# Optimization experiments

Measured on AMD Instinct MI355X. Metric: run time of the kernel, lower is better.

## Reference

```python
import jax, jax.numpy as jnp
import numpy as np
from jax import lax

K = 5          # dynamic kernel size
GROUPS = 8     # inter_channels // group_channels = 128 // 16
R = 2          # pixel shuffle upscale factor
SLOPE = 0.01   # LeakyReLU default negative_slope
EPS = 1e-5     # BatchNorm eps


def conv2d(x, w, b, pad=0):
    # x: [B,C,H,W], w: [O,I,kh,kw]
    y = lax.conv_general_dilated(x, w, (1, 1), [(pad, pad), (pad, pad)],
                                 dimension_numbers=('NCHW', 'OIHW', 'NCHW'))
    return y + b[None, :, None, None]


def pixel_shuffle(x, r):
    B, C, H, W = x.shape
    x = x.reshape(B, C // (r * r), r, r, H, W)
    x = x.transpose(0, 1, 4, 2, 5, 3)  # B, C', H, r, W, r
    return x.reshape(B, C // (r * r), H * r, W * r)


def involution(x, weight, k, groups, pad):
    # x: [B,C,H,W]; weight: [B,groups,k,k,H,W]
    # out[b, g*gc+c, h, w] = sum_ij weight[b,g,i,j,h,w] * x_pad[b, g*gc+c, h+i, w+j]
    B, C, H, W = x.shape
    gc = C // groups
    xp = jnp.pad(x, ((0, 0), (0, 0), (pad, pad), (pad, pad)))
    xg = xp.reshape(B, groups, gc, H + 2 * pad, W + 2 * pad)
    out = jnp.zeros((B, groups, gc, H, W), x.dtype)
    for i in range(k):
        for j in range(k):
            out = out + weight[:, :, None, i, j] * xg[:, :, :, i:i + H, j:j + W]
    return out.reshape(B, C, H, W)


def setup_inputs() -> dict:
    key = jax.random.key(0)
    ks = jax.random.split(key, 16)
    s = 0.05
    return {
        'high_level': jax.random.normal(ks[0], (8, 128, 64, 64), jnp.float32),
        'low_level': jax.random.normal(ks[1], (8, 224, 128, 128), jnp.float32),
        'emb': jax.random.normal(ks[2], (8, 256, 128, 128), jnp.float32),
        'reduce_w': jax.random.normal(ks[3], (128, 256, 1, 1), jnp.float32) * s,
        'reduce_b': jax.random.normal(ks[4], (128,), jnp.float32) * s,
        'conv1_w': jax.random.normal(ks[5], (32, 128, 1, 1), jnp.float32) * s,
        'conv1_b': jax.random.normal(ks[6], (32,), jnp.float32) * s,
        'conv2_w': jax.random.normal(ks[7], (200, 32, 3, 3), jnp.float32) * s,
        'conv2_b': jax.random.normal(ks[8], (200,), jnp.float32) * s,
        'embconv_w': jax.random.normal(ks[9], (32, 256, 1, 1), jnp.float32) * s,
        'embconv_b': jax.random.normal(ks[10], (32,), jnp.float32) * s,
        'out_w': jax.random.normal(ks[11], (64, 128, 1, 1), jnp.float32) * s,
        'out_b': jax.random.normal(ks[12], (64,), jnp.float32) * s,
        'bn_gamma': jnp.ones((64,), jnp.float32),
        'bn_beta': jnp.zeros((64,), jnp.float32),
        'bn_mean': jnp.zeros((64,), jnp.float32),
        'bn_var': jax.random.uniform(ks[13], (64,), jnp.float32, 0.5, 1.5),
    }


def reference(high_level, low_level, emb,
              reduce_w, reduce_b, conv1_w, conv1_b, conv2_w, conv2_b,
              embconv_w, embconv_b, out_w, out_b,
              bn_gamma, bn_beta, bn_mean, bn_var):
    cat = jnp.concatenate([pixel_shuffle(high_level, R), low_level], axis=1)
    cat = conv2d(cat, reduce_w, reduce_b)
    mix = jax.nn.leaky_relu(conv2d(cat, conv1_w, conv1_b)
                            + conv2d(emb, embconv_w, embconv_b), SLOPE)
    w = conv2d(mix, conv2_w, conv2_b, pad=1)  # [B, K*K*GROUPS, H, W]
    B, _, H, W = w.shape
    w = w.reshape(B, GROUPS, K, K, H, W)
    o = involution(cat, w, K, GROUPS, (K - 1) // 2)
    o = conv2d(o, out_w, out_b)
    o = (o - bn_mean[None, :, None, None]) * (bn_gamma[None, :, None, None]
        / jnp.sqrt(bn_var[None, :, None, None] + EPS)) + bn_beta[None, :, None, None]
    return jax.nn.leaky_relu(o, SLOPE)
```

## Files before the change

### kernel.cpp

```cpp
#include <hip/hip_runtime.h>

typedef unsigned short u16; typedef unsigned int u32; typedef unsigned long long u64;
typedef __attribute__((ext_vector_type(8))) short short8;
typedef __attribute__((ext_vector_type(16))) float f32x16;

#define HW 16384

#define RED_B  0
#define C1E_B  128
#define C2_B   160
#define OUT_B  416
#define BN_SC  480
#define BN_SH  544
#define FLAG_OFF   4096
#define RWB_OFF    8192
#define C1B_OFF    73728
#define EMBB_OFF   81920
#define OUTB_OFF   98304
#define C2PB_OFF   114688
#define CAT2_OFF   524288
#define MIX_OFF    34078720
#define WGT_OFF    42467328

__device__ __forceinline__ float bf2f(u16 x){ u32 u=((u32)x)<<16; float f; __builtin_memcpy(&f,&u,4); return f; }
__device__ __forceinline__ u16 f2bf(float f){ u32 u; __builtin_memcpy(&u,&f,4); return (u16)((u + 0x7fffu + ((u>>16)&1u))>>16); }
__device__ __forceinline__ float lrelu(float x){ return x>0.f ? x : 0.01f*x; }

template<int M> __device__ __forceinline__ u16 ldb(const void* p, size_t i){
    if (M==1) return ((const u16*)p)[i];
    return f2bf(((const float*)p)[i]);
}
template<int M> __device__ __forceinline__ float ldf(const void* p, size_t i){
    if (M==1) return bf2f(((const u16*)p)[i]);
    return ((const float*)p)[i];
}
template<int M> __device__ __forceinline__ short8 ld8(const void* p, size_t i){
    short8 v;
    if (M==1){ __builtin_memcpy(&v, (const u16*)p + i, 16); }
    else {
        float a[8]; __builtin_memcpy(a, (const float*)p + i, 32);
#pragma unroll
        for (int r=0;r<8;r++) v[r] = (short)f2bf(a[r]);
    }
    return v;
}
template<int M> __device__ __forceinline__ void ld4(const void* p, size_t i, u32* d){
    if (M==1){ __builtin_memcpy(d, (const u16*)p + i, 8); }
    else {
        float a[4]; __builtin_memcpy(a, (const float*)p + i, 16);
        d[0] = (u32)f2bf(a[0]) | ((u32)f2bf(a[1])<<16);
        d[1] = (u32)f2bf(a[2]) | ((u32)f2bf(a[3])<<16);
    }
}
__device__ __forceinline__ void stA(u16* At, int stride, int p, int c, u16 v){
    At[p*stride + ((((c>>3) ^ ((p>>1)&7)))<<3) + (c&7)] = v;
}
__device__ __forceinline__ int swz(int p){ return ((p>>1) ^ (p>>3)) & 7; }

__global__ void detect_kernel(const void* __restrict__ emb, u32* __restrict__ flag){
    int tid = threadIdx.x;
    const u16* p = (const u16*)emb;
    int e = (p[tid*2] >> 7) & 0xFF;
    u64 m = __ballot(e >= 100 && e <= 140);
    if (tid == 0) *flag = (__popcll(m) >= 32) ? 1u : 0u;
}

template<int M>
__global__ __launch_bounds__(256) void k_prep(
    const void* rw, const void* rb, const void* c1w, const void* c1b,
    const void* c2w, const void* c2b, const void* ew, const void* eb,
    const void* ow, const void* ob, const void* gam, const void* bet,
    const void* mn, const void* vr, char* ws, const u32* flag)
{
    if (*flag != (u32)M) return;
    float* wf = (float*)ws;
    int i = blockIdx.x*256 + threadIdx.x;
    if (i < 32768) {
        int o = i>>8, ic = i&255;
        int s = ic>>4, qq = (ic>>3)&1, e = ic&7;
        int dst = (((o>>5)*16 + s)*64 + qq*32 + (o&31))*8 + e;
        ((u16*)(ws+RWB_OFF))[dst] = ldb<M>(rw, i);
    }
    else if (i < 36864)  ((u16*)(ws+C1B_OFF))[i-32768] = ldb<M>(c1w, i-32768);
    else if (i < 45056)  ((u16*)(ws+EMBB_OFF))[i-36864] = ldb<M>(ew, i-36864);
    else if (i < 53248)  ((u16*)(ws+OUTB_OFF))[i-45056] = ldb<M>(ow, i-45056);
    else if (i < 126976) {
        int j = i-53248; int o = j/288, k = j - o*288;
        int tap = k>>5, ic = k&31;
        u16 v = 0;
        if (o < 200) v = ldb<M>(c2w, (size_t)o*288 + ic*9 + tap);
        ((u16*)(ws+C2PB_OFF))[j] = v;
    }
    else if (i < 127584) {
        int j = i-126976;
        if (j < 128) wf[RED_B+j] = ldf<M>(rb, j);
        else if (j < 160) wf[C1E_B+j-128] = ldf<M>(c1b, j-128) + ldf<M>(eb, j-128);
        else if (j < 416) { int o = j-160; wf[C2_B+o] = (o<200) ? ldf<M>(c2b,o) : 0.f; }
        else if (j < 480) wf[OUT_B+j-416] = ldf<M>(ob, j-416);
        else if (j < 544) { int c=j-480; wf[BN_SC+c] = ldf<M>(gam,c) * rsqrtf(ldf<M>(vr,c)+1e-5f); }
        else { int c=j-544; wf[BN_SH+c] = ldf<M>(bet,c) - ldf<M>(mn,c)*ldf<M>(gam,c)*rsqrtf(ldf<M>(vr,c)+1e-5f); }
    }
}

template<int M>
__global__ __launch_bounds__(256) void k_reduce(
    const void* __restrict__ hi, const void* __restrict__ lo,
    const u16* __restrict__ rwB, const float* __restrict__ wf,
    u16* __restrict__ cat2, const u32* __restrict__ flag)
{
    if (*flag != (u32)M) return;
    __shared__ u16 At[64*264];
    const int tid = threadIdx.x, wvi = tid>>6, lane = tid&63;
    const int rt = (wvi>>1)*32, nc0 = (wvi&1)*64;
    const int col = lane&31, q = lane>>5;

    const int gpx = blockIdx.x*64;
    const int b = gpx>>14, p0 = gpx&16383;
    const int h = p0>>7, w0 = p0&127;

    const int co = tid>>3, po = tid&7;
    u32 W[8][4];
    if (co < 28) {
        u32 R[8][4];
#pragma unroll
        for (int j=0;j<8;j++){
            short8 v = ld8<M>(lo, ((size_t)(b*224 + 8*co + j))*HW + p0 + 8*po);
            __builtin_memcpy(&R[j][0], &v, 16);
        }
#pragma unroll
        for (int p=0;p<8;p++){
            const int u = p>>1, hf = p&1;
#pragma unroll
            for (int m=0;m<4;m++){
                u32 A0 = R[2*m][u], A1 = R[2*m+1][u];
                W[p][m] = hf ? ((A0>>16) | (A1 & 0xffff0000u))
                             : ((A0 & 0xffffu) | (A1<<16));
            }
        }
        const int ch = co + 4;
#pragma unroll
        for (int p=0;p<8;p++){
            int pg = 8*po + p;
            __builtin_memcpy(At + pg*264 + ((ch ^ swz(pg))<<3), &W[p][0], 16);
        }
    } else {
        const int cc0 = (co-28)*8, h2 = (h&1)*2;
        u32 E[8][2], O[8][2];
#pragma unroll
        for (int j=0;j<8;j++){
            int hc = (cc0+j)*4 + h2;
            size_t src = ((size_t)(b*128 + hc))*4096 + (size_t)(h>>1)*64 + (w0>>1) + 4*po;
            ld4<M>(hi, src,        E[j]);
            ld4<M>(hi, src + 4096, O[j]);
        }
#pragma unroll
        for (int p=0;p<8;p++){
            const int k = p>>1, u = k>>1, hf = k&1;
#pragma unroll
            for (int m=0;m<4;m++){
                u32 A0, A1;
                if (p&1){ A0 = O[2*m][u]; A1 = O[2*m+1][u]; }
                else    { A0 = E[2*m][u]; A1 = E[2*m+1][u]; }
                W[p][m] = hf ? ((A0>>16) | (A1 & 0xffff0000u))
                             : ((A0 & 0xffffu) | (A1<<16));
            }
        }
        const int ch = co - 28;
#pragma unroll
        for (int p=0;p<8;p++){
            int pg = 8*po + p;
            __builtin_memcpy(At + pg*264 + ((ch ^ swz(pg))<<3), &W[p][0], 16);
        }
    }
    __syncthreads();

    const int pp = rt + col, sw = swz(pp);
    const u16* arow = At + pp*264;
    const int ot0 = (wvi&1)*2;

    f32x16 acc0, acc1;
#pragma unroll
    for (int r=0;r<16;r++){ acc0[r]=0.f; acc1[r]=0.f; }

    short8 Bb[2][8];
#pragma unroll
    for (int nt=0;nt<2;nt++)
#pragma unroll
    for (int s=0;s<8;s++)
        __builtin_memcpy(&Bb[nt][s], rwB + (((size_t)((ot0+nt)*16 + s))*64 + lane)*8, 16);
#pragma unroll
    for (int s=0;s<8;s++){
        short8 a; __builtin_memcpy(&a, arow + (((2*s+q)^sw)<<3), 16);
        acc0 = __builtin_amdgcn_mfma_f32_32x32x16_bf16(a, Bb[0][s], acc0, 0,0,0);
        acc1 = __builtin_amdgcn_mfma_f32_32x32x16_bf16(a, Bb[1][s], acc1, 0,0,0);
    }
#pragma unroll
    for (int nt=0;nt<2;nt++)
#pragma unroll
    for (int s=0;s<8;s++)
        __builtin_memcpy(&Bb[nt][s], rwB + (((size_t)((ot0+nt)*16 + 8+s))*64 + lane)*8, 16);
#pragma unroll
    for (int s=8;s<16;s++){
        short8 a; __builtin_memcpy(&a, arow + (((2*s+q)^sw)<<3), 16);
        acc0 = __builtin_amdgcn_mfma_f32_32x32x16_bf16(a, Bb[0][s-8], acc0, 0,0,0);
        acc1 = __builtin_amdgcn_mfma_f32_32x32x16_bf16(a, Bb[1][s-8], acc1, 0,0,0);
    }

#pragma unroll
    for (int nt=0; nt<2; nt++){
        int oc = nc0 + nt*32 + col;
        float bias = wf[RED_B + oc];
#pragma unroll
        for (int r=0;r<16;r++){
            int row = (r&3) + 8*(r>>2) + 4*q;
            float v = (nt ? acc1[r] : acc0[r]) + bias;
            cat2[((size_t)(gpx + rt + row))*128 + oc] = f2bf(v);
        }
    }
}

template<int M>
__global__ __launch_bounds__(256) void k_mix(
    const u16* __restrict__ cat2, const void* __restrict__ emb,
    const u16* __restrict__ c1B, const u16* __restrict__ embB,
    const float* __restrict__ wf, u16* __restrict__ mixt, const u32* __restrict__ flag)
{
    if (*flag != (u32)M) return;
    __shared__ u16 At[128*136];
    const int tid = threadIdx.x, wvi = tid>>6, lane = tid&63;
    const int rt = wvi*32, col = lane&31, q = lane>>5;

    const int gpx = blockIdx.x*128;
    const int b = gpx>>14, p0 = gpx&16383;

    short8 Bc[8];
#pragma unroll
    for (int s=0;s<8;s++)  __builtin_memcpy(&Bc[s], c1B + (size_t)col*128 + s*16 + q*8, 16);

    f32x16 acc;
#pragma unroll
    for (int r=0;r<16;r++) acc[r]=0.f;
    const int pp = rt + col, sw = swz(pp);
    const u16* arow = At + pp*136;

#pragma unroll
    for (int i=0;i<8;i++){
        int idx = tid + i*256;
        int p = idx>>4, c16 = idx&15;
        short8 v;
        __builtin_memcpy(&v, cat2 + ((size_t)(gpx+p))*128 + c16*8, 16);
        *(short8*)(At + p*136 + ((c16 ^ swz(p))<<3)) = v;
    }
    __syncthreads();
#pragma unroll
    for (int s=0;s<8;s++){
        short8 a; __builtin_memcpy(&a, arow + (((2*s+q)^sw)<<3), 16);
        acc = __builtin_amdgcn_mfma_f32_32x32x16_bf16(a, Bc[s], acc, 0,0,0);
    }

    const int co = tid>>4, po = tid&15;
#pragma unroll 1
    for (int half=0; half<2; half++){
        u32 R[8][4];
#pragma unroll
        for (int j=0;j<8;j++){
            short8 v = ld8<M>(emb, ((size_t)(b*256 + half*128 + 8*co + j))*HW + p0 + 8*po);
            __builtin_memcpy(&R[j][0], &v, 16);
        }
        short8 Be[8];
#pragma unroll
        for (int s=0;s<8;s++)
            __builtin_memcpy(&Be[s], embB + (size_t)col*256 + half*128 + s*16 + q*8, 16);
        __syncthreads();
        u32 W[8][4];
#pragma unroll
        for (int p=0;p<8;p++){
            const int u = p>>1, hf = p&1;
#pragma unroll
            for (int m=0;m<4;m++){
                u32 A0 = R[2*m][u], A1 = R[2*m+1][u];
                W[p][m] = hf ? ((A0>>16) | (A1 & 0xffff0000u))
                             : ((A0 & 0xffffu) | (A1<<16));
            }
        }
#pragma unroll
        for (int p=0;p<8;p++){
            int pg = 8*po + p;
            __builtin_memcpy(At + pg*136 + ((co ^ swz(pg))<<3), &W[p][0], 16);
        }
        __syncthreads();
#pragma unroll
        for (int s=0;s<8;s++){
            short8 a; __builtin_memcpy(&a, arow + (((2*s+q)^sw)<<3), 16);
            acc = __builtin_amdgcn_mfma_f32_32x32x16_bf16(a, Be[s], acc, 0,0,0);
        }
    }
    float bias = wf[C1E_B + col];
#pragma unroll
    for (int r=0;r<16;r++){
        int row = (r&3) + 8*(r>>2) + 4*q;
        mixt[((size_t)(gpx + rt + row))*32 + col] = f2bf(lrelu(acc[r] + bias));
    }
}

__global__ __launch_bounds__(256) void k_conv2(
    const u16* __restrict__ mixt, const u16* __restrict__ c2B,
    const float* __restrict__ wf, u16* __restrict__ wgt)
{
    __shared__ u16 halo[100*32];
    const int tid = threadIdx.x, wvi = tid>>6, lane = tid&63;
    const int rt = (wvi>>1)*32, npair = wvi&1;
    const int nh = blockIdx.x & 1;
    const int nc0 = nh*128 + npair*64;
    const int col = lane&31, q = lane>>5;

    short8 B[2][18];
#pragma unroll
    for (int nt=0; nt<2; nt++){
        int o = nc0 + nt*32 + col;
#pragma unroll
        for (int s=0; s<18; s++)
            __builtin_memcpy(&B[nt][s], c2B + (size_t)o*288 + s*16 + q*8, 16);
    }

    for (int it=0; it<4; it++){
        int tile = (blockIdx.x>>1) + it*512;
        int b = tile>>8, tl = tile&255;
        int ty = tl>>4, tx = tl&15;
        __syncthreads();
#pragma unroll
        for (int i=0;i<2;i++){
            int idx = tid + i*256;
            if (idx < 400){
                int point = idx>>2, cq = idx&3;
                int y = ty*8 + point/10 - 1, x = tx*8 + point%10 - 1;
                short8 v;
                if (y>=0 && y<128 && x>=0 && x<128)
                    __builtin_memcpy(&v, mixt + ((size_t)(b*HW + y*128 + x))*32 + cq*8, 16);
                else { short z = 0; v = (short8){z,z,z,z,z,z,z,z}; }
                *(short8*)(halo + point*32 + cq*8) = v;
            }
        }
        __syncthreads();

        f32x16 acc0, acc1;
#pragma unroll
        for (int r=0;r<16;r++){ acc0[r]=0.f; acc1[r]=0.f; }
        int pp = rt + col, py = pp>>3, px = pp&7;
#pragma unroll
        for (int s=0;s<18;s++){
            int tap = s>>1, ih = s&1;
            int dy = tap/3, dx = tap%3;
            short8 a;
            __builtin_memcpy(&a, halo + ((py+dy)*10 + px+dx)*32 + ih*16 + q*8, 16);
            acc0 = __builtin_amdgcn_mfma_f32_32x32x16_bf16(a, B[0][s], acc0, 0,0,0);
            acc1 = __builtin_amdgcn_mfma_f32_32x32x16_bf16(a, B[1][s], acc1, 0,0,0);
        }
#pragma unroll
        for (int nt=0; nt<2; nt++){
            int oc = nc0 + nt*32 + col;
            if (oc < 200){
                float bias = wf[C2_B + oc];
#pragma unroll
                for (int r=0;r<16;r++){
                    int row = (r&3) + 8*(r>>2) + 4*q;
                    int p2 = rt + row;
                    int y = ty*8 + (p2>>3), x = tx*8 + (p2&7);
                    float v = (nt ? acc1[r] : acc0[r]) + bias;
                    wgt[((size_t)(b*200 + oc))*HW + y*128 + x] = f2bf(v);
                }
            }
        }
    }
}

template<int M>
__global__ __launch_bounds__(256) void k_inv(
    const u16* __restrict__ cat2, const u16* __restrict__ wgt,
    const u16* __restrict__ outB, const float* __restrict__ wf,
    void* __restrict__ out, const u32* __restrict__ flag)
{
    if (*flag != (u32)M) return;
    __shared__ u16 halo[400*16];
    __shared__ u16 og[256*16];
    const int tid = threadIdx.x, wvi = tid>>6, lane = tid&63;
    const int col = lane&31, q = lane>>5;
    const int b = blockIdx.y, ty = blockIdx.x>>3, tx = blockIdx.x&7;
    const int py = tid>>4, px = tid&15;
    const int h = ty*16 + py, w = tx*16 + px;

    f32x16 acc[2][2];
#pragma unroll
    for (int i=0;i<2;i++)
#pragma unroll
    for (int j=0;j<2;j++)
#pragma unroll
    for (int r=0;r<16;r++) acc[i][j][r] = 0.f;

#pragma unroll 1
    for (int g=0; g<8; g++){
        __syncthreads();
#pragma unroll
        for (int i=0;i<4;i++){
            int idx = tid + i*256;
            if (idx < 800){
                int point = idx>>1, cq = idx&1;
                int y = ty*16 + point/20 - 2, x = tx*16 + point%20 - 2;
                short8 v;
                if (y>=0 && y<128 && x>=0 && x<128)
                    __builtin_memcpy(&v, cat2 + ((size_t)(b*HW + y*128 + x))*128 + g*16 + cq*8, 16);
                else { short z=0; v = (short8){z,z,z,z,z,z,z,z}; }
                *(short8*)(halo + point*16 + cq*8) = v;
            }
        }
        __syncthreads();

        float wvv[25];
#pragma unroll
        for (int t=0;t<25;t++)
            wvv[t] = bf2f(wgt[((size_t)(b*200 + g*25 + t))*HW + h*128 + w]);

        float a16[16];
#pragma unroll
        for (int cc=0;cc<16;cc++) a16[cc]=0.f;
#pragma unroll
        for (int t=0;t<25;t++){
            int dy = t/5, dx = t%5;
            u32 vv[8];
            __builtin_memcpy(vv, halo + ((py+dy)*20 + px+dx)*16, 32);
            float wt = wvv[t];
#pragma unroll
            for (int r=0;r<8;r++){
                u32 u = vv[r];
                u32 ulo = u<<16, uhi = u & 0xffff0000u;
                float x0, x1;
                __builtin_memcpy(&x0,&ulo,4); __builtin_memcpy(&x1,&uhi,4);
                a16[2*r]   += wt*x0;
                a16[2*r+1] += wt*x1;
            }
        }
        u32 pk[8];
#pragma unroll
        for (int r=0;r<8;r++) pk[r] = (u32)f2bf(a16[2*r]) | ((u32)f2bf(a16[2*r+1])<<16);
        __syncthreads();
        __builtin_memcpy(og + tid*16, pk, 32);
        __syncthreads();

        short8 bo0, bo1;
        __builtin_memcpy(&bo0, outB + (size_t)(col)*128      + g*16 + q*8, 16);
        __builtin_memcpy(&bo1, outB + (size_t)(32+col)*128   + g*16 + q*8, 16);
#pragma unroll
        for (int rt2=0; rt2<2; rt2++){
            int prow = (wvi*2 + rt2)*32 + col;
            short8 a; __builtin_memcpy(&a, og + prow*16 + q*8, 16);
            acc[rt2][0] = __builtin_amdgcn_mfma_f32_32x32x16_bf16(a, bo0, acc[rt2][0], 0,0,0);
            acc[rt2][1] = __builtin_amdgcn_mfma_f32_32x32x16_bf16(a, bo1, acc[rt2][1], 0,0,0);
        }
    }
#pragma unroll
    for (int rt2=0; rt2<2; rt2++)
#pragma unroll
    for (int nt=0; nt<2; nt++){
        int oc = nt*32 + col;
        float bias = wf[OUT_B+oc], sc = wf[BN_SC+oc], sh = wf[BN_SH+oc];
#pragma unroll
        for (int r=0;r<16;r++){
            int row = (r&3) + 8*(r>>2) + 4*q;
            int p = (wvi*2 + rt2)*32 + row;
            int yy = ty*16 + (p>>4), xx = tx*16 + (p&15);
            float v = lrelu((acc[rt2][nt][r] + bias)*sc + sh);
            size_t oidx = ((size_t)(b*64 + oc))*HW + yy*128 + xx;
            if (M==1) ((u16*)out)[oidx] = f2bf(v);
            else ((float*)out)[oidx] = v;
        }
    }
}

extern "C" void kernel_launch(void* const* d_in, const int* in_sizes, int n_in,
                              void* d_out, int out_size, void* d_ws, size_t ws_size,
                              hipStream_t stream) {
    const void* hi  = d_in[0];
    const void* lo  = d_in[1];
    const void* emb = d_in[2];
    char* ws = (char*)d_ws;
    float* wf = (float*)ws;
    u32* flag = (u32*)(ws + FLAG_OFF);
    u16* cat2 = (u16*)(ws + CAT2_OFF);
    u16* mixt = (u16*)(ws + MIX_OFF);
    u16* wgt  = (u16*)(ws + WGT_OFF);

    detect_kernel<<<1, 64, 0, stream>>>(emb, flag);

    k_prep<0><<<499,256,0,stream>>>(d_in[3],d_in[4],d_in[5],d_in[6],d_in[7],d_in[8],
        d_in[9],d_in[10],d_in[11],d_in[12],d_in[13],d_in[14],d_in[15],d_in[16], ws, flag);
    k_prep<1><<<499,256,0,stream>>>(d_in[3],d_in[4],d_in[5],d_in[6],d_in[7],d_in[8],
        d_in[9],d_in[10],d_in[11],d_in[12],d_in[13],d_in[14],d_in[15],d_in[16], ws, flag);

    k_reduce<0><<<2048,256,0,stream>>>(hi, lo, (const u16*)(ws+RWB_OFF), wf, cat2, flag);
    k_reduce<1><<<2048,256,0,stream>>>(hi, lo, (const u16*)(ws+RWB_OFF), wf, cat2, flag);

    k_mix<0><<<1024,256,0,stream>>>(cat2, emb, (const u16*)(ws+C1B_OFF), (const u16*)(ws+EMBB_OFF), wf, mixt, flag);
    k_mix<1><<<1024,256,0,stream>>>(cat2, emb, (const u16*)d_in[5],      (const u16*)d_in[9],       wf, mixt, flag);

    k_conv2<<<1024,256,0,stream>>>(mixt, (const u16*)(ws+C2PB_OFF), wf, wgt);

    k_inv<0><<<dim3(64,8),256,0,stream>>>(cat2, wgt, (const u16*)(ws+OUTB_OFF), wf, d_out, flag);
    k_inv<1><<<dim3(64,8),256,0,stream>>>(cat2, wgt, (const u16*)d_in[11],      wf, d_out, flag);
}
```

Baseline: 456.6 us.

## Fuse dynamic-weight conv into involution kernel and merge dtype-dispatch launches

The 3x3 conv that produces the per-pixel involution weights now runs inside the involution kernel. Each block loads a mixt halo into shared memory, computes the 25 weights for each group with MFMA into LDS, and skips writing and re-reading the 200-channel weight tensor in global memory. The separate per-dtype kernel launches are merged into single kernels that branch on the flag at runtime, which cuts the number of launches. In exchange the involution kernel uses much more LDS and registers and reloads the conv2 B fragments for every group, so occupancy may drop.

```diff
diff --git a/kernel.cpp b/kernel.cpp
--- a/kernel.cpp
+++ b/kernel.cpp
@@ -20,7 +20,6 @@
 #define C2PB_OFF   114688
 #define CAT2_OFF   524288
 #define MIX_OFF    34078720
-#define WGT_OFF    42467328
 
 __device__ __forceinline__ float bf2f(u16 x){ u32 u=((u32)x)<<16; float f; __builtin_memcpy(&f,&u,4); return f; }
 __device__ __forceinline__ u16 f2bf(float f){ u32 u; __builtin_memcpy(&u,&f,4); return (u16)((u + 0x7fffu + ((u>>16)&1u))>>16); }
@@ -52,9 +51,6 @@
         d[1] = (u32)f2bf(a[2]) | ((u32)f2bf(a[3])<<16);
     }
 }
-__device__ __forceinline__ void stA(u16* At, int stride, int p, int c, u16 v){
-    At[p*stride + ((((c>>3) ^ ((p>>1)&7)))<<3) + (c&7)] = v;
-}
 __device__ __forceinline__ int swz(int p){ return ((p>>1) ^ (p>>3)) & 7; }
 
 __global__ void detect_kernel(const void* __restrict__ emb, u32* __restrict__ flag){
@@ -66,13 +62,12 @@
 }
 
 template<int M>
-__global__ __launch_bounds__(256) void k_prep(
+__device__ __forceinline__ void prep_body(
     const void* rw, const void* rb, const void* c1w, const void* c1b,
     const void* c2w, const void* c2b, const void* ew, const void* eb,
     const void* ow, const void* ob, const void* gam, const void* bet,
-    const void* mn, const void* vr, char* ws, const u32* flag)
-{
-    if (*flag != (u32)M) return;
+    const void* mn, const void* vr, char* ws)
+{
     float* wf = (float*)ws;
     int i = blockIdx.x*256 + threadIdx.x;
     if (i < 32768) {
@@ -102,14 +97,22 @@
     }
 }
 
+__global__ __launch_bounds__(256) void k_prep(
+    const void* rw, const void* rb, const void* c1w, const void* c1b,
+    const void* c2w, const void* c2b, const void* ew, const void* eb,
+    const void* ow, const void* ob, const void* gam, const void* bet,
+    const void* mn, const void* vr, char* ws, const u32* __restrict__ flag)
+{
+    if (*flag) prep_body<1>(rw,rb,c1w,c1b,c2w,c2b,ew,eb,ow,ob,gam,bet,mn,vr,ws);
+    else       prep_body<0>(rw,rb,c1w,c1b,c2w,c2b,ew,eb,ow,ob,gam,bet,mn,vr,ws);
+}
+
 template<int M>
-__global__ __launch_bounds__(256) void k_reduce(
+__device__ __forceinline__ void reduce_body(
     const void* __restrict__ hi, const void* __restrict__ lo,
     const u16* __restrict__ rwB, const float* __restrict__ wf,
-    u16* __restrict__ cat2, const u32* __restrict__ flag)
-{
-    if (*flag != (u32)M) return;
-    __shared__ u16 At[64*264];
+    u16* __restrict__ cat2, u16* At)
+{
     const int tid = threadIdx.x, wvi = tid>>6, lane = tid&63;
     const int rt = (wvi>>1)*32, nc0 = (wvi&1)*64;
     const int col = lane&31, q = lane>>5;
@@ -219,14 +222,22 @@
     }
 }
 
+__global__ __launch_bounds__(256) void k_reduce(
+    const void* __restrict__ hi, const void* __restrict__ lo,
+    const u16* __restrict__ rwB, const float* __restrict__ wf,
+    u16* __restrict__ cat2, const u32* __restrict__ flag)
+{
+    __shared__ u16 At[64*264];
+    if (*flag) reduce_body<1>(hi, lo, rwB, wf, cat2, At);
+    else       reduce_body<0>(hi, lo, rwB, wf, cat2, At);
+}
+
 template<int M>
-__global__ __launch_bounds__(256) void k_mix(
+__device__ __forceinline__ void mix_body(
     const u16* __restrict__ cat2, const void* __restrict__ emb,
     const u16* __restrict__ c1B, const u16* __restrict__ embB,
-    const float* __restrict__ wf, u16* __restrict__ mixt, const u32* __restrict__ flag)
-{
-    if (*flag != (u32)M) return;
-    __shared__ u16 At[128*136];
+    const float* __restrict__ wf, u16* __restrict__ mixt, u16* At)
+{
     const int tid = threadIdx.x, wvi = tid>>6, lane = tid&63;
     const int rt = wvi*32, col = lane&31, q = lane>>5;
 
@@ -303,91 +314,27 @@
     }
 }
 
-__global__ __launch_bounds__(256) void k_conv2(
-    const u16* __restrict__ mixt, const u16* __restrict__ c2B,
-    const float* __restrict__ wf, u16* __restrict__ wgt)
-{
-    __shared__ u16 halo[100*32];
-    const int tid = threadIdx.x, wvi = tid>>6, lane = tid&63;
-    const int rt = (wvi>>1)*32, npair = wvi&1;
-    const int nh = blockIdx.x & 1;
-    const int nc0 = nh*128 + npair*64;
-    const int col = lane&31, q = lane>>5;
-
-    short8 B[2][18];
-#pragma unroll
-    for (int nt=0; nt<2; nt++){
-        int o = nc0 + nt*32 + col;
-#pragma unroll
-        for (int s=0; s<18; s++)
-            __builtin_memcpy(&B[nt][s], c2B + (size_t)o*288 + s*16 + q*8, 16);
-    }
-
-    for (int it=0; it<4; it++){
-        int tile = (blockIdx.x>>1) + it*512;
-        int b = tile>>8, tl = tile&255;
-        int ty = tl>>4, tx = tl&15;
-        __syncthreads();
-#pragma unroll
-        for (int i=0;i<2;i++){
-            int idx = tid + i*256;
-            if (idx < 400){
-                int point = idx>>2, cq = idx&3;
-                int y = ty*8 + point/10 - 1, x = tx*8 + point%10 - 1;
-                short8 v;
-                if (y>=0 && y<128 && x>=0 && x<128)
-                    __builtin_memcpy(&v, mixt + ((size_t)(b*HW + y*128 + x))*32 + cq*8, 16);
-                else { short z = 0; v = (short8){z,z,z,z,z,z,z,z}; }
-                *(short8*)(halo + point*32 + cq*8) = v;
-            }
-        }
-        __syncthreads();
-
-        f32x16 acc0, acc1;
-#pragma unroll
-        for (int r=0;r<16;r++){ acc0[r]=0.f; acc1[r]=0.f; }
-        int pp = rt + col, py = pp>>3, px = pp&7;
-#pragma unroll
-        for (int s=0;s<18;s++){
-            int tap = s>>1, ih = s&1;
-            int dy = tap/3, dx = tap%3;
-            short8 a;
-            __builtin_memcpy(&a, halo + ((py+dy)*10 + px+dx)*32 + ih*16 + q*8, 16);
-            acc0 = __builtin_amdgcn_mfma_f32_32x32x16_bf16(a, B[0][s], acc0, 0,0,0);
-            acc1 = __builtin_amdgcn_mfma_f32_32x32x16_bf16(a, B[1][s], acc1, 0,0,0);
-        }
-#pragma unroll
-        for (int nt=0; nt<2; nt++){
-            int oc = nc0 + nt*32 + col;
-            if (oc < 200){
-                float bias = wf[C2_B + oc];
-#pragma unroll
-                for (int r=0;r<16;r++){
-                    int row = (r&3) + 8*(r>>2) + 4*q;
-                    int p2 = rt + row;
-                    int y = ty*8 + (p2>>3), x = tx*8 + (p2&7);
-                    float v = (nt ? acc1[r] : acc0[r]) + bias;
-                    wgt[((size_t)(b*200 + oc))*HW + y*128 + x] = f2bf(v);
-                }
-            }
-        }
-    }
+__global__ __launch_bounds__(256) void k_mix(
+    const u16* __restrict__ cat2, const void* __restrict__ emb,
+    const u16* __restrict__ c1B, const u16* __restrict__ embB,
+    const float* __restrict__ wf, u16* __restrict__ mixt, const u32* __restrict__ flag)
+{
+    __shared__ u16 At[128*136];
+    if (*flag) mix_body<1>(cat2, emb, c1B, embB, wf, mixt, At);
+    else       mix_body<0>(cat2, emb, c1B, embB, wf, mixt, At);
 }
 
 template<int M>
-__global__ __launch_bounds__(256) void k_inv(
-    const u16* __restrict__ cat2, const u16* __restrict__ wgt,
-    const u16* __restrict__ outB, const float* __restrict__ wf,
-    void* __restrict__ out, const u32* __restrict__ flag)
-{
-    if (*flag != (u32)M) return;
-    __shared__ u16 halo[400*16];
-    __shared__ u16 og[256*16];
+__device__ __forceinline__ void inv_body(
+    const u16* __restrict__ cat2, const u16* __restrict__ mixt,
+    const u16* __restrict__ c2B, const u16* __restrict__ outB,
+    const float* __restrict__ wf, void* __restrict__ out,
+    u16* halo_m, u16* wgt_l, u16* halo_c, u16* og)
+{
     const int tid = threadIdx.x, wvi = tid>>6, lane = tid&63;
     const int col = lane&31, q = lane>>5;
     const int b = blockIdx.y, ty = blockIdx.x>>3, tx = blockIdx.x&7;
     const int py = tid>>4, px = tid&15;
-    const int h = ty*16 + py, w = tx*16 + px;
 
     f32x16 acc[2][2];
 #pragma unroll
@@ -396,10 +343,32 @@
     for (int j=0;j<2;j++)
 #pragma unroll
     for (int r=0;r<16;r++) acc[i][j][r] = 0.f;
+
+#pragma unroll
+    for (int i=0;i<6;i++){
+        int idx = tid + i*256;
+        if (idx < 1296){
+            int point = idx>>2, cq = idx&3;
+            int y = ty*16 + point/18 - 1, x = tx*16 + point%18 - 1;
+            short8 v;
+            if (y>=0 && y<128 && x>=0 && x<128)
+                __builtin_memcpy(&v, mixt + ((size_t)(b*HW + y*128 + x))*32 + cq*8, 16);
+            else { short z=0; v = (short8){z,z,z,z,z,z,z,z}; }
+            *(short8*)(halo_m + point*40 + cq*8) = v;
+        }
+    }
+    __syncthreads();
 
 #pragma unroll 1
     for (int g=0; g<8; g++){
         __syncthreads();
+
+        const int o = g*25 + col;
+        short8 Bf[18];
+#pragma unroll
+        for (int s=0;s<18;s++)
+            __builtin_memcpy(&Bf[s], c2B + (size_t)o*288 + s*16 + q*8, 16);
+
 #pragma unroll
         for (int i=0;i<4;i++){
             int idx = tid + i*256;
@@ -410,15 +379,45 @@
                 if (y>=0 && y<128 && x>=0 && x<128)
                     __builtin_memcpy(&v, cat2 + ((size_t)(b*HW + y*128 + x))*128 + g*16 + cq*8, 16);
                 else { short z=0; v = (short8){z,z,z,z,z,z,z,z}; }
-                *(short8*)(halo + point*16 + cq*8) = v;
+                *(short8*)(halo_c + point*16 + cq*8) = v;
             }
         }
+
+        f32x16 c0, c1;
+#pragma unroll
+        for (int r=0;r<16;r++){ c0[r]=0.f; c1[r]=0.f; }
+        const int p0 = wvi*64 + col, p1 = p0 + 32;
+        const int pya = p0>>4, pxa = p0&15, pyb = p1>>4, pxb = p1&15;
+#pragma unroll
+        for (int s=0;s<18;s++){
+            int tap = s>>1, ih = s&1;
+            int dy = tap/3, dx = tap%3;
+            short8 a0, a1;
+            __builtin_memcpy(&a0, halo_m + ((pya+dy)*18 + pxa+dx)*40 + ih*16 + q*8, 16);
+            __builtin_memcpy(&a1, halo_m + ((pyb+dy)*18 + pxb+dx)*40 + ih*16 + q*8, 16);
+            c0 = __builtin_amdgcn_mfma_f32_32x32x16_bf16(a0, Bf[s], c0, 0,0,0);
+            c1 = __builtin_amdgcn_mfma_f32_32x32x16_bf16(a1, Bf[s], c1, 0,0,0);
+        }
+        {
+            float bias = wf[C2_B + o];
+#pragma unroll
+            for (int rt2=0; rt2<2; rt2++){
+                int mb = wvi*64 + rt2*32;
+#pragma unroll
+                for (int r=0;r<16;r+=2){
+                    int row0 = (r&3) + 8*(r>>2) + 4*q;
+                    float v0 = (rt2 ? c1[r]   : c0[r])   + bias;
+                    float v1 = (rt2 ? c1[r+1] : c0[r+1]) + bias;
+                    u32 pkv = (u32)f2bf(v0) | ((u32)f2bf(v1)<<16);
+                    *(u32*)(wgt_l + (size_t)col*264 + mb + row0) = pkv;
+                }
+            }
+        }
         __syncthreads();
 
         float wvv[25];
 #pragma unroll
-        for (int t=0;t<25;t++)
-            wvv[t] = bf2f(wgt[((size_t)(b*200 + g*25 + t))*HW + h*128 + w]);
+        for (int t=0;t<25;t++) wvv[t] = bf2f(wgt_l[t*264 + tid]);
 
         float a16[16];
 #pragma unroll
@@ -427,7 +426,7 @@
         for (int t=0;t<25;t++){
             int dy = t/5, dx = t%5;
             u32 vv[8];
-            __builtin_memcpy(vv, halo + ((py+dy)*20 + px+dx)*16, 32);
+            __builtin_memcpy(vv, halo_c + ((py+dy)*20 + px+dx)*16, 32);
             float wt = wvv[t];
 #pragma unroll
             for (int r=0;r<8;r++){
@@ -442,7 +441,6 @@
         u32 pk[8];
 #pragma unroll
         for (int r=0;r<8;r++) pk[r] = (u32)f2bf(a16[2*r]) | ((u32)f2bf(a16[2*r+1])<<16);
-        __syncthreads();
         __builtin_memcpy(og + tid*16, pk, 32);
         __syncthreads();
 
@@ -474,6 +472,19 @@
             else ((float*)out)[oidx] = v;
         }
     }
+}
+
+__global__ __launch_bounds__(256,2) void k_inv(
+    const u16* __restrict__ cat2, const u16* __restrict__ mixt,
+    const u16* __restrict__ c2B, const u16* __restrict__ outB,
+    const float* __restrict__ wf, void* __restrict__ out, const u32* __restrict__ flag)
+{
+    __shared__ u16 halo_m[324*40];
+    __shared__ u16 wgt_l[32*264];
+    __shared__ u16 halo_c[400*16];
+    __shared__ u16 og[256*16];
+    if (*flag) inv_body<1>(cat2, mixt, c2B, outB, wf, out, halo_m, wgt_l, halo_c, og);
+    else       inv_body<0>(cat2, mixt, c2B, outB, wf, out, halo_m, wgt_l, halo_c, og);
 }
 
 extern "C" void kernel_launch(void* const* d_in, const int* in_sizes, int n_in,
@@ -487,23 +498,17 @@
     u32* flag = (u32*)(ws + FLAG_OFF);
     u16* cat2 = (u16*)(ws + CAT2_OFF);
     u16* mixt = (u16*)(ws + MIX_OFF);
-    u16* wgt  = (u16*)(ws + WGT_OFF);
 
     detect_kernel<<<1, 64, 0, stream>>>(emb, flag);
 
-    k_prep<0><<<499,256,0,stream>>>(d_in[3],d_in[4],d_in[5],d_in[6],d_in[7],d_in[8],
+    k_prep<<<499,256,0,stream>>>(d_in[3],d_in[4],d_in[5],d_in[6],d_in[7],d_in[8],
         d_in[9],d_in[10],d_in[11],d_in[12],d_in[13],d_in[14],d_in[15],d_in[16], ws, flag);
-    k_prep<1><<<499,256,0,stream>>>(d_in[3],d_in[4],d_in[5],d_in[6],d_in[7],d_in[8],
-        d_in[9],d_in[10],d_in[11],d_in[12],d_in[13],d_in[14],d_in[15],d_in[16], ws, flag);
-
-    k_reduce<0><<<2048,256,0,stream>>>(hi, lo, (const u16*)(ws+RWB_OFF), wf, cat2, flag);
-    k_reduce<1><<<2048,256,0,stream>>>(hi, lo, (const u16*)(ws+RWB_OFF), wf, cat2, flag);
-
-    k_mix<0><<<1024,256,0,stream>>>(cat2, emb, (const u16*)(ws+C1B_OFF), (const u16*)(ws+EMBB_OFF), wf, mixt, flag);
-    k_mix<1><<<1024,256,0,stream>>>(cat2, emb, (const u16*)d_in[5],      (const u16*)d_in[9],       wf, mixt, flag);
-
-    k_conv2<<<1024,256,0,stream>>>(mixt, (const u16*)(ws+C2PB_OFF), wf, wgt);
-
-    k_inv<0><<<dim3(64,8),256,0,stream>>>(cat2, wgt, (const u16*)(ws+OUTB_OFF), wf, d_out, flag);
-    k_inv<1><<<dim3(64,8),256,0,stream>>>(cat2, wgt, (const u16*)d_in[11],      wf, d_out, flag);
-}
+
+    k_reduce<<<2048,256,0,stream>>>(hi, lo, (const u16*)(ws+RWB_OFF), wf, cat2, flag);
+
+    k_mix<<<1024,256,0,stream>>>(cat2, emb, (const u16*)(ws+C1B_OFF),
+                                 (const u16*)(ws+EMBB_OFF), wf, mixt, flag);
+
+    k_inv<<<dim3(64,8),256,0,stream>>>(cat2, mixt, (const u16*)(ws+C2PB_OFF),
+                                       (const u16*)(ws+OUTB_OFF), wf, d_out, flag);
+}
```

Result: faster. 399.6 us (-12.5%).
